# Optimization experiments

Hardware: AMD Instinct MI355X
Metric: run time of the kernel (lower is better)

## Reference

```python
import jax, jax.numpy as jnp
import numpy as np

H0, H1, NHID, BATCH = 256, 256, 512, 2048

def setup_inputs() -> dict:
    key = jax.random.key(0)
    k1, k2, k3, k4, k5 = jax.random.split(key, 5)
    initrange = 0.1
    inputs = jax.random.normal(k1, (BATCH, NHID), dtype=jnp.float32)
    labels = jax.random.randint(k2, (BATCH,), 0, H1, dtype=jnp.int32)
    parent_labels = jax.random.randint(k3, (BATCH,), 0, H0, dtype=jnp.int32)
    layer_top_W = jax.random.uniform(k4, (NHID, H0), jnp.float32, -initrange, initrange)
    layer_top_b = jnp.zeros((H0,), jnp.float32)
    layer_bottom_W = jax.random.uniform(k5, (H0, NHID, H1), jnp.float32, -initrange, initrange)
    layer_bottom_b = jnp.zeros((H0, H1), jnp.float32)
    return {"inputs": inputs, "labels": labels, "parent_labels": parent_labels,
            "layer_top_W": layer_top_W, "layer_top_b": layer_top_b,
            "layer_bottom_W": layer_bottom_W, "layer_bottom_b": layer_bottom_b}

def reference(inputs, labels, parent_labels, layer_top_W, layer_top_b,
              layer_bottom_W, layer_bottom_b):
    batch = inputs.shape[0]
    # top-level softmax over coarse classes: [B, H0]
    top_probs = jax.nn.softmax(inputs @ layer_top_W + layer_top_b, axis=1)
    # per-sample gather of expert weight slice [B, NHID, H1] then bmm
    Wb = layer_bottom_W[parent_labels]            # [B, NHID, H1]
    bb = layer_bottom_b[parent_labels]            # [B, H1]
    bottom_logits = jnp.einsum('bd,bdk->bk', inputs, Wb) + bb
    bottom_probs = jax.nn.softmax(bottom_logits, axis=1)
    ar = jnp.arange(batch)
    target_probs = top_probs[ar, parent_labels] * bottom_probs[ar, labels]
    return target_probs
```

## Files before the change

kernel.cpp:

```cpp
#include <hip/hip_runtime.h>

constexpr int BATCH = 2048;
constexpr int NHID  = 512;
constexpr int H0    = 256;
constexpr int H1    = 256;
constexpr int S     = 8;
constexpr int J     = 3;

__global__ __launch_bounds__(128) void hs_8s(
    const float* __restrict__ x,
    const int*   __restrict__ labels,
    const int*   __restrict__ parents,
    const float* __restrict__ topW,
    const float* __restrict__ topb,
    const float* __restrict__ botW,
    const float* __restrict__ botb,
    float*       __restrict__ out)
{
    const int p = blockIdx.x / J;
    const int j = blockIdx.x % J;
    const int t = threadIdx.x;
    const int g = t >> 6;
    const int l = t & 63;

    __shared__ int   list[BATCH];
    __shared__ int   wcnt[2];
    __shared__ __align__(16) float xs[S][NHID];
    __shared__ float psm[2][S];

    int running = 0;
    for (int c = 0; c < BATCH; c += 128) {
        const bool match = (parents[c + t] == p);
        const unsigned long long mask = __ballot(match);
        if (l == 0) wcnt[g] = __popcll(mask);
        __syncthreads();
        const int off = running + (g ? wcnt[0] : 0);
        if (match)
            list[off + __popcll(mask & ((1ull << l) - 1ull))] = c + t;
        running += wcnt[0] + wcnt[1];
        __syncthreads();
    }
    const int n = running;
    if (n <= j * S) return;

    const float* Wbase = g ? botW + (size_t)p * NHID * H1 : topW;
    const float4 b4    = g ? *(const float4*)(botb + (size_t)p * H1 + 4 * l)
                           : *(const float4*)(topb + 4 * l);

    for (int base = j * S; base < n; base += J * S) {
        const int rem = min(S, n - base);

        for (int s = 0; s < S; ++s) {
            const int idx = list[base + min(s, rem - 1)];
            ((float4*)xs[s])[t] = ((const float4*)(x + (size_t)idx * NHID))[t];
        }

        int tgts[S];
        #pragma unroll
        for (int s = 0; s < S; ++s) {
            const int slot = base + min(s, rem - 1);
            tgts[s] = g ? labels[list[slot]] : p;
        }
        __syncthreads();

        float4 acc[S];
        #pragma unroll
        for (int s = 0; s < S; ++s) acc[s] = make_float4(0.f, 0.f, 0.f, 0.f);

        const float* Wp = Wbase + 4 * l;
        float4 ring[8];
        #pragma unroll
        for (int i = 0; i < 8; ++i)
            ring[i] = *(const float4*)(Wp + (size_t)i * H0);

        for (int d = 0; d < NHID; d += 8) {
            #pragma unroll
            for (int h = 0; h < 2; ++h) {
                const int dd = d + 4 * h;
                const float4 w0 = ring[4 * h + 0], w1 = ring[4 * h + 1];
                const float4 w2 = ring[4 * h + 2], w3 = ring[4 * h + 3];
                if (dd + 8 < NHID) {
                    #pragma unroll
                    for (int i = 0; i < 4; ++i)
                        ring[4 * h + i] =
                            *(const float4*)(Wp + (size_t)(dd + 8 + i) * H0);
                }
                #pragma unroll
                for (int s = 0; s < S; ++s) {
                    const float4 xv = *(const float4*)&xs[s][dd];
                    float4 a = acc[s];
                    a.x = fmaf(xv.x, w0.x, a.x); a.y = fmaf(xv.x, w0.y, a.y);
                    a.z = fmaf(xv.x, w0.z, a.z); a.w = fmaf(xv.x, w0.w, a.w);
                    a.x = fmaf(xv.y, w1.x, a.x); a.y = fmaf(xv.y, w1.y, a.y);
                    a.z = fmaf(xv.y, w1.z, a.z); a.w = fmaf(xv.y, w1.w, a.w);
                    a.x = fmaf(xv.z, w2.x, a.x); a.y = fmaf(xv.z, w2.y, a.y);
                    a.z = fmaf(xv.z, w2.z, a.z); a.w = fmaf(xv.z, w2.w, a.w);
                    a.x = fmaf(xv.w, w3.x, a.x); a.y = fmaf(xv.w, w3.y, a.y);
                    a.z = fmaf(xv.w, w3.z, a.z); a.w = fmaf(xv.w, w3.w, a.w);
                    acc[s] = a;
                }
            }
        }

        #pragma unroll
        for (int s = 0; s < S; ++s) {
            float4 v = acc[s];
            v.x += b4.x; v.y += b4.y; v.z += b4.z; v.w += b4.w;

            float m = fmaxf(fmaxf(v.x, v.y), fmaxf(v.z, v.w));
            #pragma unroll
            for (int off = 32; off > 0; off >>= 1)
                m = fmaxf(m, __shfl_xor(m, off, 64));

            const float ex = expf(v.x - m), ey = expf(v.y - m);
            const float ez = expf(v.z - m), ew = expf(v.w - m);
            float sum = (ex + ey) + (ez + ew);
            #pragma unroll
            for (int off = 32; off > 0; off >>= 1)
                sum += __shfl_xor(sum, off, 64);

            const int tgt = tgts[s];
            const int k   = tgt & 3;
            const float ev = (k == 0) ? ex : (k == 1) ? ey : (k == 2) ? ez : ew;
            if (l == (tgt >> 2))
                psm[g][s] = ev / sum;
        }
        __syncthreads();

        if (t < rem) {
            const int idx = list[base + t];
            out[idx] = psm[0][t] * psm[1][t];
        }
        __syncthreads();
    }
}

extern "C" void kernel_launch(void* const* d_in, const int* in_sizes, int n_in,
                              void* d_out, int out_size, void* d_ws, size_t ws_size,
                              hipStream_t stream) {
    const float* x       = (const float*)d_in[0];
    const int*   labels  = (const int*)  d_in[1];
    const int*   parents = (const int*)  d_in[2];
    const float* topW    = (const float*)d_in[3];
    const float* topb    = (const float*)d_in[4];
    const float* botW    = (const float*)d_in[5];
    const float* botb    = (const float*)d_in[6];
    float*       out     = (float*)d_out;

    hs_8s<<<H0 * J, 128, 0, stream>>>(x, labels, parents,
                                      topW, topb, botW, botb, out);
}
```

Before: 228.8 us.

## Replace FP32 FMA kernel with split-bf16 MFMA per-parent batched GEMM

Rewrites the kernel so each block handles one parent class with 512 threads and processes up to 32 samples at once. The top and bottom matmuls are computed with bf16 MFMA instructions using a hi/lo split (three MFMAs per tile) to approximate fp32 accuracy. Weights are staged through swizzled shared memory with a register prefetch, and both softmaxes then run from shared memory. This removes the scalar FMA bottleneck and the redundant weight re-reads across the J sub-blocks, at the cost of extra conversion work, much more LDS, lower occupancy, and small precision differences.

```diff
diff --git a/kernel.cpp b/kernel.cpp
--- a/kernel.cpp
+++ b/kernel.cpp
@@ -4,10 +4,21 @@
 constexpr int NHID  = 512;
 constexpr int H0    = 256;
 constexpr int H1    = 256;
-constexpr int S     = 8;
-constexpr int J     = 3;
-
-__global__ __launch_bounds__(128) void hs_8s(
+constexpr int SMAX  = 32;
+constexpr int KC    = 32;
+constexpr int NKC   = NHID / KC;
+
+typedef __attribute__((ext_vector_type(8))) short short8v;
+typedef __attribute__((ext_vector_type(4))) float f32x4;
+
+static __device__ __forceinline__ unsigned short bf_hi(float f) {
+    return (unsigned short)(__float_as_uint(f) >> 16);
+}
+static __device__ __forceinline__ float bf_f(unsigned short h) {
+    return __uint_as_float(((unsigned int)h) << 16);
+}
+
+__global__ __launch_bounds__(512) void hs_mfma(
     const float* __restrict__ x,
     const int*   __restrict__ labels,
     const int*   __restrict__ parents,
@@ -17,119 +28,200 @@
     const float* __restrict__ botb,
     float*       __restrict__ out)
 {
-    const int p = blockIdx.x / J;
-    const int j = blockIdx.x % J;
+    const int p = blockIdx.x;
     const int t = threadIdx.x;
     const int g = t >> 6;
     const int l = t & 63;
 
-    __shared__ int   list[BATCH];
-    __shared__ int   wcnt[2];
-    __shared__ __align__(16) float xs[S][NHID];
-    __shared__ float psm[2][S];
+    __shared__ int list[BATCH];
+    __shared__ int wcnt[8];
+    __shared__ __align__(16) unsigned short Ahi[SMAX * NHID];
+    __shared__ __align__(16) unsigned short Alo[SMAX * NHID];
+    __shared__ __align__(16) float Bf[KC * NHID];
 
     int running = 0;
-    for (int c = 0; c < BATCH; c += 128) {
+    for (int c = 0; c < BATCH; c += 512) {
         const bool match = (parents[c + t] == p);
         const unsigned long long mask = __ballot(match);
         if (l == 0) wcnt[g] = __popcll(mask);
         __syncthreads();
-        const int off = running + (g ? wcnt[0] : 0);
+        int off = running;
+        #pragma unroll
+        for (int w = 0; w < 8; ++w) {
+            const int cw = wcnt[w];
+            if (w < g) off += cw;
+            running += cw;
+        }
         if (match)
             list[off + __popcll(mask & ((1ull << l) - 1ull))] = c + t;
-        running += wcnt[0] + wcnt[1];
         __syncthreads();
     }
     const int n = running;
-    if (n <= j * S) return;
-
-    const float* Wbase = g ? botW + (size_t)p * NHID * H1 : topW;
-    const float4 b4    = g ? *(const float4*)(botb + (size_t)p * H1 + 4 * l)
-                           : *(const float4*)(topb + 4 * l);
-
-    for (int base = j * S; base < n; base += J * S) {
-        const int rem = min(S, n - base);
-
-        for (int s = 0; s < S; ++s) {
-            const int idx = list[base + min(s, rem - 1)];
-            ((float4*)xs[s])[t] = ((const float4*)(x + (size_t)idx * NHID))[t];
-        }
-
-        int tgts[S];
-        #pragma unroll
-        for (int s = 0; s < S; ++s) {
-            const int slot = base + min(s, rem - 1);
-            tgts[s] = g ? labels[list[slot]] : p;
-        }
-        __syncthreads();
-
-        float4 acc[S];
-        #pragma unroll
-        for (int s = 0; s < S; ++s) acc[s] = make_float4(0.f, 0.f, 0.f, 0.f);
-
-        const float* Wp = Wbase + 4 * l;
-        float4 ring[8];
-        #pragma unroll
-        for (int i = 0; i < 8; ++i)
-            ring[i] = *(const float4*)(Wp + (size_t)i * H0);
-
-        for (int d = 0; d < NHID; d += 8) {
-            #pragma unroll
-            for (int h = 0; h < 2; ++h) {
-                const int dd = d + 4 * h;
-                const float4 w0 = ring[4 * h + 0], w1 = ring[4 * h + 1];
-                const float4 w2 = ring[4 * h + 2], w3 = ring[4 * h + 3];
-                if (dd + 8 < NHID) {
-                    #pragma unroll
-                    for (int i = 0; i < 4; ++i)
-                        ring[4 * h + i] =
-                            *(const float4*)(Wp + (size_t)(dd + 8 + i) * H0);
-                }
-                #pragma unroll
-                for (int s = 0; s < S; ++s) {
-                    const float4 xv = *(const float4*)&xs[s][dd];
-                    float4 a = acc[s];
-                    a.x = fmaf(xv.x, w0.x, a.x); a.y = fmaf(xv.x, w0.y, a.y);
-                    a.z = fmaf(xv.x, w0.z, a.z); a.w = fmaf(xv.x, w0.w, a.w);
-                    a.x = fmaf(xv.y, w1.x, a.x); a.y = fmaf(xv.y, w1.y, a.y);
-                    a.z = fmaf(xv.y, w1.z, a.z); a.w = fmaf(xv.y, w1.w, a.w);
-                    a.x = fmaf(xv.z, w2.x, a.x); a.y = fmaf(xv.z, w2.y, a.y);
-                    a.z = fmaf(xv.z, w2.z, a.z); a.w = fmaf(xv.z, w2.w, a.w);
-                    a.x = fmaf(xv.w, w3.x, a.x); a.y = fmaf(xv.w, w3.y, a.y);
-                    a.z = fmaf(xv.w, w3.z, a.z); a.w = fmaf(xv.w, w3.w, a.w);
-                    acc[s] = a;
-                }
-            }
-        }
-
-        #pragma unroll
-        for (int s = 0; s < S; ++s) {
-            float4 v = acc[s];
-            v.x += b4.x; v.y += b4.y; v.z += b4.z; v.w += b4.w;
-
-            float m = fmaxf(fmaxf(v.x, v.y), fmaxf(v.z, v.w));
-            #pragma unroll
-            for (int off = 32; off > 0; off >>= 1)
-                m = fmaxf(m, __shfl_xor(m, off, 64));
-
-            const float ex = expf(v.x - m), ey = expf(v.y - m);
-            const float ez = expf(v.z - m), ew = expf(v.w - m);
-            float sum = (ex + ey) + (ez + ew);
-            #pragma unroll
-            for (int off = 32; off > 0; off >>= 1)
-                sum += __shfl_xor(sum, off, 64);
-
-            const int tgt = tgts[s];
-            const int k   = tgt & 3;
-            const float ev = (k == 0) ? ex : (k == 1) ? ey : (k == 2) ? ez : ew;
-            if (l == (tgt >> 2))
-                psm[g][s] = ev / sum;
-        }
-        __syncthreads();
-
-        if (t < rem) {
-            const int idx = list[base + t];
-            out[idx] = psm[0][t] * psm[1][t];
+    if (n == 0) return;
+
+    const float4 bb = *(const float4*)(botb + (size_t)p * H1 + 4 * l);
+    const float4 bt = *(const float4*)(topb + 4 * l);
+
+    const int r   = g & 1;
+    const int ctb = (g >> 1) * 8;
+    const int sk  = t >> 4;
+    const int sc  = 4 * (t & 15);
+    const float* bW = botW + (size_t)p * NHID * H1;
+
+    for (int base = 0; base < n; base += SMAX) {
+        const int rem = min(SMAX, n - base);
+
+        {
+            const int s  = t >> 4;
+            const int c0 = 32 * (t & 15);
+            const float* xr =
+                x + (size_t)list[base + min(s, rem - 1)] * NHID + c0;
+            #pragma unroll
+            for (int b = 0; b < 4; ++b) {
+                const float4 v0 = ((const float4*)xr)[2 * b];
+                const float4 v1 = ((const float4*)xr)[2 * b + 1];
+                const float fe[8] = {v0.x, v0.y, v0.z, v0.w,
+                                     v1.x, v1.y, v1.z, v1.w};
+                short8v hv, lv;
+                #pragma unroll
+                for (int e = 0; e < 8; ++e) {
+                    const unsigned short h = bf_hi(fe[e]);
+                    hv[e] = (short)h;
+                    lv[e] = (short)bf_hi(fe[e] - bf_f(h));
+                }
+                const int byte = ((s * NHID + c0 + 8 * b) * 2) ^ ((s & 7) << 4);
+                *(short8v*)((char*)Ahi + byte) = hv;
+                *(short8v*)((char*)Alo + byte) = lv;
+            }
+        }
+
+        f32x4 acc[8];
+        #pragma unroll
+        for (int i = 0; i < 8; ++i) acc[i] = (f32x4)(0.0f);
+
+        float4 sreg[8];
+        __syncthreads();
+
+        {
+            const float* bsrc = bW + (size_t)sk * H1 + sc;
+            const float* tsrc = topW + (size_t)sk * H0 + sc;
+            #pragma unroll
+            for (int i = 0; i < 4; ++i) {
+                sreg[i]     = *(const float4*)(bsrc + 64 * i);
+                sreg[4 + i] = *(const float4*)(tsrc + 64 * i);
+            }
+        }
+
+        for (int kc = 0; kc < NKC; ++kc) {
+            __syncthreads();
+            #pragma unroll
+            for (int i = 0; i < 8; ++i) {
+                const int c    = sc + 64 * i;
+                const int byte = ((sk * NHID + c) * 4) ^ ((sk & 7) << 4);
+                *(float4*)((char*)Bf + byte) = sreg[i];
+            }
+            __syncthreads();
+
+            if (kc + 1 < NKC) {
+                const int k0 = (kc + 1) * KC + sk;
+                const float* bsrc = bW + (size_t)k0 * H1 + sc;
+                const float* tsrc = topW + (size_t)k0 * H0 + sc;
+                #pragma unroll
+                for (int i = 0; i < 4; ++i) {
+                    sreg[i]     = *(const float4*)(bsrc + 64 * i);
+                    sreg[4 + i] = *(const float4*)(tsrc + 64 * i);
+                }
+            }
+
+            const int K0   = kc * KC;
+            const int arow = 16 * r + (l & 15);
+            const int ab   = ((arow * NHID + K0 + (l >> 4) * 8) * 2)
+                             ^ ((arow & 7) << 4);
+            const short8v af_h = *(const short8v*)((const char*)Ahi + ab);
+            const short8v af_l = *(const short8v*)((const char*)Alo + ab);
+
+            #pragma unroll
+            for (int i = 0; i < 8; ++i) {
+                const int cB = 16 * (ctb + i) + (l & 15);
+                float bfv[8];
+                #pragma unroll
+                for (int e = 0; e < 8; ++e) {
+                    const int kk   = (l >> 4) * 8 + e;
+                    const int byte = ((kk * NHID + cB) * 4) ^ ((kk & 7) << 4);
+                    bfv[e] = *(const float*)((const char*)Bf + byte);
+                }
+                short8v bh, bl;
+                #pragma unroll
+                for (int e = 0; e < 8; ++e) {
+                    const unsigned short h = bf_hi(bfv[e]);
+                    bh[e] = (short)h;
+                    bl[e] = (short)bf_hi(bfv[e] - bf_f(h));
+                }
+                acc[i] = __builtin_amdgcn_mfma_f32_16x16x32_bf16(
+                             af_h, bh, acc[i], 0, 0, 0);
+                acc[i] = __builtin_amdgcn_mfma_f32_16x16x32_bf16(
+                             af_l, bh, acc[i], 0, 0, 0);
+                acc[i] = __builtin_amdgcn_mfma_f32_16x16x32_bf16(
+                             af_h, bl, acc[i], 0, 0, 0);
+            }
+        }
+
+        __syncthreads();
+        #pragma unroll
+        for (int i = 0; i < 8; ++i) {
+            const int col = 16 * (ctb + i) + (l & 15);
+            #pragma unroll
+            for (int j = 0; j < 4; ++j) {
+                const int row = 16 * r + (l >> 4) * 4 + j;
+                Bf[row * NHID + col] = acc[i][j];
+            }
+        }
+        __syncthreads();
+
+        #pragma unroll
+        for (int i = 0; i < 4; ++i) {
+            const int s = 4 * g + i;
+            if (s < rem) {
+                const int idx = list[base + s];
+                const float* Lrow = Bf + s * NHID;
+
+                float4 v = *(const float4*)(Lrow + 4 * l);
+                v.x += bb.x; v.y += bb.y; v.z += bb.z; v.w += bb.w;
+                float m = fmaxf(fmaxf(v.x, v.y), fmaxf(v.z, v.w));
+                #pragma unroll
+                for (int off = 32; off > 0; off >>= 1)
+                    m = fmaxf(m, __shfl_xor(m, off, 64));
+                const float ex = expf(v.x - m), ey = expf(v.y - m);
+                const float ez = expf(v.z - m), ew = expf(v.w - m);
+                float sum = (ex + ey) + (ez + ew);
+                #pragma unroll
+                for (int off = 32; off > 0; off >>= 1)
+                    sum += __shfl_xor(sum, off, 64);
+                const int tb_ = labels[idx];
+                const int kb_ = tb_ & 3;
+                const float evb = (kb_ == 0) ? ex : (kb_ == 1) ? ey
+                                : (kb_ == 2) ? ez : ew;
+                const float pb = __shfl(evb / sum, tb_ >> 2, 64);
+
+                float4 u = *(const float4*)(Lrow + 256 + 4 * l);
+                u.x += bt.x; u.y += bt.y; u.z += bt.z; u.w += bt.w;
+                float mu = fmaxf(fmaxf(u.x, u.y), fmaxf(u.z, u.w));
+                #pragma unroll
+                for (int off = 32; off > 0; off >>= 1)
+                    mu = fmaxf(mu, __shfl_xor(mu, off, 64));
+                const float tx = expf(u.x - mu), ty = expf(u.y - mu);
+                const float tz = expf(u.z - mu), tw = expf(u.w - mu);
+                float tsum = (tx + ty) + (tz + tw);
+                #pragma unroll
+                for (int off = 32; off > 0; off >>= 1)
+                    tsum += __shfl_xor(tsum, off, 64);
+                const int kt_ = p & 3;
+                const float evt = (kt_ == 0) ? tx : (kt_ == 1) ? ty
+                                : (kt_ == 2) ? tz : tw;
+                const float pt = __shfl(evt / tsum, p >> 2, 64);
+
+                if (l == 0) out[idx] = pt * pb;
+            }
         }
         __syncthreads();
     }
@@ -147,6 +239,6 @@
     const float* botb    = (const float*)d_in[6];
     float*       out     = (float*)d_out;
 
-    hs_8s<<<H0 * J, 128, 0, stream>>>(x, labels, parents,
-                                      topW, topb, botW, botb, out);
-}
+    hs_mfma<<<H0, 512, 0, stream>>>(x, labels, parents,
+                                    topW, topb, botW, botb, out);
+}
```

Result: slower. 322.5 us (+41.0%).
